# Performance work log

Measured on AMD Instinct MI355X. Metric: run time of the kernel, lower is better.

Reference implementation:

```python
import jax, jax.numpy as jnp
import numpy as np

B_SZ = 4; SEQ = 2048; D_INPUT = 40; D_MODEL = 128; N_LAYERS = 4
D_STATE = 16; EXPAND = 2; D_INNER = D_MODEL * EXPAND
N_HEADS = 4; D_HEAD = D_MODEL // N_HEADS; MAX_LANDMARKS = 100
EPS_RMS = 1.1920929e-07  # torch nn.RMSNorm default eps = finfo(float32).eps
EPS_LN = 1e-5
A_FLOOR = 1e-4


def _rms(x, w):
    return x * jax.lax.rsqrt(jnp.mean(x * x, -1, keepdims=True) + EPS_RMS) * w


def _ln(x, w, b):
    m = jnp.mean(x, -1, keepdims=True)
    v = jnp.mean((x - m) ** 2, -1, keepdims=True)
    return (x - m) * jax.lax.rsqrt(v + EPS_LN) * w + b


def _mamba3_block(xin, Wi, Wx, Wdt, bdt, Alog, Bb, Cb, Bnw, Cnw, rf, Dv, Wo):
    # xin: (B,L,d_model)
    xz = xin @ Wi                       # (B,L,2*d_inner)
    xp, z = jnp.split(xz, 2, axis=-1)
    xp = jax.nn.silu(xp)
    sp = xp @ Wx                        # (B,L,2*d_state+2)
    B_raw = sp[..., :D_STATE]
    C_raw = sp[..., D_STATE:2 * D_STATE]
    dt_in = sp[..., -2:-1]
    lam_in = sp[..., -1:]
    Bm = _rms(B_raw + Bb, Bnw)
    Cm = _rms(C_raw + Cb, Cnw)
    dt = jax.nn.softplus(dt_in @ Wdt + bdt)   # (B,L,d_inner)
    lam = jax.nn.sigmoid(lam_in)              # (B,L,1)
    # data-dependent RoPE on B and C
    freqs = jax.nn.softplus(rf)                                  # (d_state//2,)
    ang = jnp.cumsum(jnp.mean(dt, -1, keepdims=True), axis=1) * freqs  # (B,L,ds/2)
    ca, sa = jnp.cos(ang), jnp.sin(ang)

    def rot(M):
        e, o = M[..., ::2], M[..., 1::2]
        return jnp.stack([e * ca - o * sa, e * sa + o * ca], -1).reshape(M.shape)

    Bm, Cm = rot(Bm), rot(Cm)
    A = jnp.minimum(-jnp.exp(Alog), -A_FLOOR)   # (d_inner,d_state)
    dte = dt[..., None]                          # (B,L,d_inner,1)
    dA = jnp.exp(A * dte)                        # (B,L,d_inner,d_state)
    Bx = Bm[:, :, None, :] * xp[..., None]       # (B,L,d_inner,d_state)
    Bx_prev = jnp.concatenate([jnp.zeros_like(Bx[:, :1]), Bx[:, :-1]], axis=1)
    lame = lam[..., None]                        # (B,L,1,1)
    u = (1.0 - lame) * dte * dA * Bx_prev + lame * dte * Bx
    u = u.at[:, 0].set(dte[:, 0] * Bx[:, 0])     # t==0 case: h = dt*B*x (no lambda)

    def step(h, inp):
        dA_t, u_t, C_t = inp
        h = dA_t * h + u_t
        return h, jnp.sum(h * C_t[:, None, :], -1)

    h0 = jnp.zeros((xin.shape[0], D_INNER, D_STATE), xin.dtype)
    _, ys = jax.lax.scan(step, h0, (jnp.swapaxes(dA, 0, 1), jnp.swapaxes(u, 0, 1), jnp.swapaxes(Cm, 0, 1)))
    y = jnp.swapaxes(ys, 0, 1)                   # (B,L,d_inner)
    y = y + xp * Dv
    y = y * jax.nn.silu(z)
    return y @ Wo


def _landmark_attn(mo, skip, hw, WQ, bQ, WK, bK, WV, bV, WO, bO):
    Bsz, L, Dm = skip.shape
    k = min(MAX_LANDMARKS, L)
    _, idx = jax.lax.top_k(hw, k)
    idx = jnp.sort(idx, axis=1)                            # (B,k)
    kv = jnp.take_along_axis(skip, idx[..., None], axis=1)  # (B,k,Dm)
    q = mo[:, -1:, :]                                       # (B,1,Dm)
    Q = (q @ WQ + bQ).reshape(Bsz, 1, N_HEADS, D_HEAD).transpose(0, 2, 1, 3)
    K = (kv @ WK + bK).reshape(Bsz, k, N_HEADS, D_HEAD).transpose(0, 2, 1, 3)
    V = (kv @ WV + bV).reshape(Bsz, k, N_HEADS, D_HEAD).transpose(0, 2, 1, 3)
    scores = jnp.einsum('bhqd,bhkd->bhqk', Q, K) * (D_HEAD ** -0.5)
    probs = jax.nn.softmax(scores, axis=-1)
    out = jnp.einsum('bhqk,bhkd->bhqd', probs, V).transpose(0, 2, 1, 3).reshape(Bsz, Dm)
    return out @ WO + bO


def setup_inputs() -> dict:
    key = jax.random.key(0)
    ks = iter(jax.random.split(key, 64))

    def nrm(shape, s=0.02):
        return jax.random.normal(next(ks), shape, jnp.float32) * s

    nl, ds, di, dm = N_LAYERS, D_STATE, D_INNER, D_MODEL
    inp = {}
    inp['x'] = jax.random.normal(next(ks), (B_SZ, SEQ, D_INPUT), jnp.float32)
    inp['hawkes_weights'] = jax.random.uniform(next(ks), (B_SZ, SEQ), jnp.float32)
    inp['emb_W'] = nrm((D_INPUT, dm)); inp['emb_b'] = jnp.zeros(dm, jnp.float32)
    inp['skip_W'] = nrm((D_INPUT, dm)); inp['skip_b'] = jnp.zeros(dm, jnp.float32)
    inp['in_proj_W'] = nrm((nl, dm, 2 * di))
    inp['x_proj_W'] = nrm((nl, di, 2 * ds + 2))
    inp['dt_proj_W'] = nrm((nl, 1, di), 1.0)
    inp['dt_proj_b'] = jnp.full((nl, di), -1.0, jnp.float32)
    inp['A_log'] = jnp.broadcast_to(jnp.log(jnp.arange(1, ds + 1, dtype=jnp.float32)), (nl, di, ds)) * jnp.ones((nl, di, ds), jnp.float32)
    inp['B_bias'] = jnp.ones((nl, ds), jnp.float32)
    inp['C_bias'] = jnp.ones((nl, ds), jnp.float32)
    inp['Bn_w'] = jnp.ones((nl, ds), jnp.float32)
    inp['Cn_w'] = jnp.ones((nl, ds), jnp.float32)
    inp['rope_freqs'] = nrm((nl, ds // 2), 0.01)
    inp['D_param'] = jnp.ones((nl, di), jnp.float32)
    inp['out_proj_W'] = nrm((nl, di, dm))
    inp['ln_w'] = jnp.ones((nl, dm), jnp.float32); inp['ln_b'] = jnp.zeros((nl, dm), jnp.float32)
    inp['fn_w'] = jnp.ones(dm, jnp.float32); inp['fn_b'] = jnp.zeros(dm, jnp.float32)
    for nm in ('Q', 'K', 'V', 'O'):
        inp['W' + nm] = nrm((dm, dm)); inp['b' + nm] = jnp.zeros(dm, jnp.float32)
    return inp


def reference(x, hawkes_weights, emb_W, emb_b, skip_W, skip_b, in_proj_W, x_proj_W,
              dt_proj_W, dt_proj_b, A_log, B_bias, C_bias, Bn_w, Cn_w, rope_freqs,
              D_param, out_proj_W, ln_w, ln_b, fn_w, fn_b, WQ, bQ, WK, bK, WV, bV, WO, bO):
    w = hawkes_weights[..., None]
    h = (x @ emb_W + emb_b) * w          # Hawkes-damped embedding for Mamba path
    skip = (x @ skip_W + skip_b) * w     # Hawkes skip for attention KV
    for i in range(N_LAYERS):
        h = h + _mamba3_block(_ln(h, ln_w[i], ln_b[i]), in_proj_W[i], x_proj_W[i],
                              dt_proj_W[i], dt_proj_b[i], A_log[i], B_bias[i], C_bias[i],
                              Bn_w[i], Cn_w[i], rope_freqs[i], D_param[i], out_proj_W[i])
    mo = _ln(h, fn_w, fn_b)
    return _landmark_attn(mo, skip, hawkes_weights, WQ, bQ, WK, bK, WV, bV, WO, bO)
```

## Files before the change

### kernel.cpp

```cpp
#include <hip/hip_runtime.h>
#include <hip/hip_fp16.h>
#include <math.h>

#define BSZ   4
#define SEQL  2048
#define DIN   40
#define DM    128
#define DI    256
#define DS    16
#define NL    4
#define NHEAD 4
#define DHEAD 32
#define KLM   100
#define NC    128
#define TC    16
#define NROWS 8
#define EROWS 16

__device__ __forceinline__ float rcp_(float x){ return __builtin_amdgcn_rcpf(x); }
__device__ __forceinline__ float sigmoidf_(float x){ return rcp_(1.0f + __expf(-x)); }
__device__ __forceinline__ float siluf_(float x){ return x*rcp_(1.0f + __expf(-x)); }
__device__ __forceinline__ float softplusf_(float x){ return fmaxf(x,0.0f) + __logf(1.0f + __expf(-fabsf(x))); }

__device__ __forceinline__ void load8(const float* p, float* r){
  const float4* q = (const float4*)p;
  float4 a=q[0], b=q[1];
  r[0]=a.x;r[1]=a.y;r[2]=a.z;r[3]=a.w; r[4]=b.x;r[5]=b.y;r[6]=b.z;r[7]=b.w;
}
__device__ __forceinline__ void store8(float* p, const float* r){
  float4* q = (float4*)p;
  q[0]=make_float4(r[0],r[1],r[2],r[3]);  q[1]=make_float4(r[4],r[5],r[6],r[7]);
}
__device__ __forceinline__ void load16(const float* p, float* r){
  load8(p, r); load8(p+8, r+8);
}
__device__ __forceinline__ void store16(float* p, const float* r){
  store8(p, r); store8(p+8, r+8);
}

__global__ __launch_bounds__(256) void convw_kernel(
    const float* __restrict__ inW, const float* __restrict__ outW,
    __half* __restrict__ Wih, __half* __restrict__ Woh)
{
  const int i = blockIdx.x*256 + threadIdx.x;
  if (i < NL*DM*2*DI) Wih[i] = __float2half_rn(inW[i]);
  if (i < NL*DI*DM)   Woh[i] = __float2half_rn(outW[i]);
}

__global__ __launch_bounds__(256) void topk_kernel(
    const float* __restrict__ hw, int* __restrict__ idxl_g)
{
  __shared__ int redcnt[2][4];
  __shared__ int eqc[8][4], gtc[8][4];

  const int b = blockIdx.x;
  const int t = threadIdx.x;
  const int lane = t & 63, w = t >> 6;

  const float* hwp = hw + (size_t)b*SEQL;
  unsigned vb[8];
  #pragma unroll
  for (int q=0;q<8;q++) vb[q] = __float_as_uint(hwp[q*256 + t]);

  unsigned kth = 0u;
  for (int bit=31; bit>=0; --bit){
    const unsigned cand = kth | (1u << bit);
    int c0 = 0;
    #pragma unroll
    for (int q=0;q<8;q++) c0 += __popcll(__ballot(vb[q] >= cand));
    const int par = bit & 1;
    if (lane == 0) redcnt[par][w] = c0;
    __syncthreads();
    const int tot = redcnt[par][0]+redcnt[par][1]+redcnt[par][2]+redcnt[par][3];
    if (tot >= KLM) kth = cand;
  }

  unsigned long long beq[8], bgt[8];
  #pragma unroll
  for (int q=0;q<8;q++){
    beq[q] = __ballot(vb[q] == kth);
    bgt[q] = __ballot(vb[q] >  kth);
  }
  if (lane == 0){
    #pragma unroll
    for (int q=0;q<8;q++){ eqc[q][w] = __popcll(beq[q]); gtc[q][w] = __popcll(bgt[q]); }
  }
  __syncthreads();
  {
    int gtTot = 0;
    #pragma unroll
    for (int q=0;q<8;q++) gtTot += gtc[q][0]+gtc[q][1]+gtc[q][2]+gtc[q][3];
    const int need_eq = KLM - gtTot;
    const unsigned long long lmask = (lane==0) ? 0ull : ((~0ull) >> (64-lane));
    int eqPfx = 0, gtPfx = 0;
    #pragma unroll
    for (int q=0;q<8;q++){
      int eqWP = 0, gtWP = 0;
      for (int w2=0; w2<w; ++w2){ eqWP += eqc[q][w2]; gtWP += gtc[q][w2]; }
      const int eqBefore = eqPfx + eqWP + __popcll(beq[q] & lmask);
      const int gtBefore = gtPfx + gtWP + __popcll(bgt[q] & lmask);
      if (vb[q] > kth){
        const int pos = gtBefore + min(eqBefore, need_eq);
        if (pos < KLM) idxl_g[b*KLM + pos] = q*256 + t;
      } else if (vb[q] == kth && eqBefore < need_eq){
        const int pos = gtBefore + eqBefore;
        if (pos < KLM) idxl_g[b*KLM + pos] = q*256 + t;
      }
      eqPfx += eqc[q][0]+eqc[q][1]+eqc[q][2]+eqc[q][3];
      gtPfx += gtc[q][0]+gtc[q][1]+gtc[q][2]+gtc[q][3];
    }
  }
}

__global__ __launch_bounds__(256) void embed_kernel(
    const float* __restrict__ x, const float* __restrict__ hw,
    const float* __restrict__ eW, const float* __restrict__ eb,
    const float* __restrict__ sW, const float* __restrict__ sb,
    float* __restrict__ hb, float* __restrict__ sk)
{
  __shared__ float xr[EROWS][DIN];
  const int t = threadIdx.x;
  const size_t R0 = (size_t)blockIdx.x * EROWS;
  for (int e=t; e<EROWS*DIN; e+=256) ((float*)xr)[e] = x[R0*DIN + e];
  __syncthreads();
  const int c = t & (DM-1), g = t >> 7;
  float ae[8], as[8];
  #pragma unroll
  for (int j=0;j<8;j++){ ae[j]=0.0f; as[j]=0.0f; }
  for (int k=0;k<DIN;k++){
    const float we  = eW[(size_t)k*DM + c];
    const float ws_ = sW[(size_t)k*DM + c];
    #pragma unroll
    for (int j=0;j<8;j++){
      const float xv = xr[g*8+j][k];
      ae[j] = fmaf(xv, we, ae[j]);
      as[j] = fmaf(xv, ws_, as[j]);
    }
  }
  const float ebv = eb[c], sbv = sb[c];
  #pragma unroll
  for (int j=0;j<8;j++){
    const size_t R = R0 + g*8 + j;
    const float w = hw[R];
    hb[R*DM + c] = (ae[j]+ebv)*w;
    sk[R*DM + c] = (as[j]+sbv)*w;
  }
}

__global__ __launch_bounds__(256) void pre_kernel(
    const float* __restrict__ hb,
    const __half* __restrict__ Wih, const float* __restrict__ Wx,
    const float* __restrict__ Wdt, const float* __restrict__ bdt,
    const float* __restrict__ Bb, const float* __restrict__ Cb,
    const float* __restrict__ Bnw, const float* __restrict__ Cnw,
    const float* __restrict__ lnw, const float* __restrict__ lnb,
    __half* __restrict__ xph, __half* __restrict__ zsh,
    float* __restrict__ dtin, float* __restrict__ Shalf,
    float* __restrict__ Bmb, float* __restrict__ Cmb,
    float* __restrict__ lamb, float* __restrict__ mdtb)
{
  __shared__ float xin[NROWS][DM+4];
  __shared__ float xps[NROWS][DI+4];
  __shared__ float spl[NROWS][40];
  __shared__ float pr[NROWS][4];

  const int t = threadIdx.x;
  const size_t R0 = (size_t)blockIdx.x * NROWS;

  {
    const int r = t >> 5, j = t & 31;
    const float4 v = ((const float4*)(hb + (R0 + r)*DM))[j];
    float s = v.x+v.y+v.z+v.w;
    #pragma unroll
    for (int o=16;o>0;o>>=1) s += __shfl_xor(s,o,32);
    const float m = s*(1.0f/DM);
    const float dx=v.x-m, dy=v.y-m, dz=v.z-m, dw=v.w-m;
    float ss = dx*dx+dy*dy+dz*dz+dw*dw;
    #pragma unroll
    for (int o=16;o>0;o>>=1) ss += __shfl_xor(ss,o,32);
    const float inv = 1.0f/sqrtf(ss*(1.0f/DM) + 1e-5f);
    const int c = j*4;
    xin[r][c+0] = dx*inv*lnw[c+0] + lnb[c+0];
    xin[r][c+1] = dy*inv*lnw[c+1] + lnb[c+1];
    xin[r][c+2] = dz*inv*lnw[c+2] + lnb[c+2];
    xin[r][c+3] = dw*inv*lnw[c+3] + lnb[c+3];
  }
  __syncthreads();

  {
    float2 a[NROWS];
    #pragma unroll
    for (int r=0;r<NROWS;r++){ a[r].x=0.0f; a[r].y=0.0f; }
    const __half2* Wc = (const __half2*)Wih + t;
    for (int k=0;k<DM;k+=4){
      const float2 w0 = __half22float2(Wc[(size_t)(k+0)*(DI)]);
      const float2 w1 = __half22float2(Wc[(size_t)(k+1)*(DI)]);
      const float2 w2 = __half22float2(Wc[(size_t)(k+2)*(DI)]);
      const float2 w3 = __half22float2(Wc[(size_t)(k+3)*(DI)]);
      #pragma unroll
      for (int r=0;r<NROWS;r++){
        const float4 xv = *(const float4*)&xin[r][k];
        a[r].x = fmaf(xv.x,w0.x,a[r].x); a[r].y = fmaf(xv.x,w0.y,a[r].y);
        a[r].x = fmaf(xv.y,w1.x,a[r].x); a[r].y = fmaf(xv.y,w1.y,a[r].y);
        a[r].x = fmaf(xv.z,w2.x,a[r].x); a[r].y = fmaf(xv.z,w2.y,a[r].y);
        a[r].x = fmaf(xv.w,w3.x,a[r].x); a[r].y = fmaf(xv.w,w3.y,a[r].y);
      }
    }
    if (t < 128){
      #pragma unroll
      for (int r=0;r<NROWS;r++){
        const float sx = siluf_(a[r].x), sy = siluf_(a[r].y);
        xps[r][2*t] = sx; xps[r][2*t+1] = sy;
        *(__half2*)&xph[(R0+r)*DI + 2*t] =
            __halves2half2(__float2half_rn(sx), __float2half_rn(sy));
      }
    } else {
      const int zc = 2*t - 2*DI + DI;
      #pragma unroll
      for (int r=0;r<NROWS;r++){
        const float sx = siluf_(a[r].x), sy = siluf_(a[r].y);
        *(__half2*)&zsh[(R0+r)*DI + zc] =
            __halves2half2(__float2half_rn(sx), __float2half_rn(sy));
      }
    }
  }
  __syncthreads();

  if (t < 136){
    const int r = t & 7, op = t >> 3;
    float ax=0.0f, ay=0.0f;
    for (int k=0;k<DI;k+=4){
      const float4 xv = *(const float4*)&xps[r][k];
      const float2 w0 = *(const float2*)&Wx[(size_t)(k+0)*34 + 2*op];
      const float2 w1 = *(const float2*)&Wx[(size_t)(k+1)*34 + 2*op];
      const float2 w2 = *(const float2*)&Wx[(size_t)(k+2)*34 + 2*op];
      const float2 w3 = *(const float2*)&Wx[(size_t)(k+3)*34 + 2*op];
      ax = fmaf(xv.x,w0.x,ax); ay = fmaf(xv.x,w0.y,ay);
      ax = fmaf(xv.y,w1.x,ax); ay = fmaf(xv.y,w1.y,ay);
      ax = fmaf(xv.z,w2.x,ax); ay = fmaf(xv.z,w2.y,ay);
      ax = fmaf(xv.w,w3.x,ax); ay = fmaf(xv.w,w3.y,ay);
    }
    spl[r][2*op] = ax; spl[r][2*op+1] = ay;
  }
  __syncthreads();

  {
    const int half = t >> 7;
    const int r2 = (t >> 4) & 7, s2 = t & 15;
    const float* bias = half ? Cb : Bb;
    const float* wn   = half ? Cnw : Bnw;
    const float v = spl[r2][half*DS + s2] + bias[s2];
    float ss = v*v;
    #pragma unroll
    for (int o=8;o>0;o>>=1) ss += __shfl_xor(ss,o,16);
    const float inv = 1.0f/sqrtf(ss*(1.0f/DS) + 1.1920929e-07f);
    (half ? Cmb : Bmb)[(R0+r2)*DS + s2] = v*inv*wn[s2];
  }

  {
    const int lane = t & 63, w = t >> 6;
    const float wdt = Wdt[t], bdtv = bdt[t];
    float Sd = 0.0f;
    #pragma unroll
    for (int r=0;r<NROWS;r++){
      const float dval = softplusf_(fmaf(spl[r][32], wdt, bdtv));
      Sd += dval;
      float s = dval;
      #pragma unroll
      for (int o=32;o>0;o>>=1) s += __shfl_xor(s,o,64);
      if (lane==0) pr[r][w] = s;
    }
    Shalf[(size_t)blockIdx.x * DI + t] = Sd;
    if (t < NROWS){
      lamb[R0+t] = sigmoidf_(spl[t][33]);
      dtin[R0+t] = spl[t][32];
    }
  }
  __syncthreads();
  if (t < NROWS)
    mdtb[R0+t] = (pr[t][0]+pr[t][1]+pr[t][2]+pr[t][3])*(1.0f/DI);
}

__global__ __launch_bounds__(256) void cumsum_kernel(
    const float* __restrict__ mdt, double* __restrict__ csum_g)
{
  __shared__ double wsum[4];
  const int b = blockIdx.x, t = threadIdx.x;
  const int lane = t & 63, w = t >> 6;
  const float* p = mdt + (size_t)b*SEQL + (size_t)t*8;
  double v[8]; double s = 0.0;
  #pragma unroll
  for (int q=0;q<8;q++){ v[q] = (double)p[q]; s += v[q]; }
  double sc = s;
  #pragma unroll
  for (int o=1;o<64;o<<=1){
    const double nb = __shfl_up(sc, o, 64);
    if (lane >= o) sc += nb;
  }
  if (lane==63) wsum[w] = sc;
  __syncthreads();
  double woff = 0.0;
  for (int j=0;j<w;j++) woff += wsum[j];
  double run = woff + sc - s;
  double* dst = csum_g + (size_t)b*SEQL + (size_t)t*8;
  #pragma unroll
  for (int q=0;q<8;q++){ run += v[q]; dst[q] = run; }
}

__global__ __launch_bounds__(256) void csfill_kernel(
    const double* __restrict__ csum_g, const float* __restrict__ rf,
    float2* __restrict__ cst)
{
  __shared__ double fqs[8];
  const int t = threadIdx.x;
  if (t < 8){
    const double xfr = (double)rf[t];
    fqs[t] = fmax(xfr, 0.0) + log1p(exp(-fabs(xfr)));
  }
  __syncthreads();
  const int row = blockIdx.x*256 + t;
  const double ab = csum_g[row];
  const double TWO_PI = 6.283185307179586;
  const double INV2PI = 0.15915494309189535;
  float2 o8[8];
  #pragma unroll
  for (int f=0; f<8; f++){
    const double ang = ab * fqs[f];
    const double red = ang - floor(ang*INV2PI)*TWO_PI;
    float sa, ca;
    __sincosf((float)red, &sa, &ca);
    o8[f] = make_float2(ca, sa);
  }
  float4* dst = (float4*)&cst[(size_t)row*8];
  dst[0] = make_float4(o8[0].x,o8[0].y,o8[1].x,o8[1].y);
  dst[1] = make_float4(o8[2].x,o8[2].y,o8[3].x,o8[3].y);
  dst[2] = make_float4(o8[4].x,o8[4].y,o8[5].x,o8[5].y);
  dst[3] = make_float4(o8[6].x,o8[6].y,o8[7].x,o8[7].y);
}

__global__ __launch_bounds__(512) void scan1_kernel(
    const __half* __restrict__ xph, const float* __restrict__ dtin,
    const float* __restrict__ Wdt, const float* __restrict__ bdt,
    const float* __restrict__ Bmb, const float* __restrict__ lamb,
    const float2* __restrict__ cst,
    const float* __restrict__ Alog, float* __restrict__ hend)
{
  __shared__ float Bst[TC+1][DS];
  __shared__ float lst[TC];
  __shared__ float dsl[TC];
  __shared__ __half xpl[TC+1][DI+8];
  const int t = threadIdx.x;
  const int d  = t >> 1;
  const int s0 = (t & 1) * 8;
  const int c = blockIdx.x & (NC-1);
  const int b = blockIdx.x >> 7;
  const size_t bL = (size_t)b*SEQL;
  const int t0 = c*TC;
  const int id = blockIdx.x*256 + d;

  for (int e=t; e<(TC+1)*DS; e+=512){
    const int j = e >> 4, s = e & 15;
    const int trow = t0 - 1 + j;
    Bst[j][s] = (trow >= 0) ? Bmb[(bL + trow)*DS + s] : 0.0f;
  }
  for (int e=t; e<(TC+1)*DI; e+=512){
    const int j = e >> 8, dd = e & (DI-1);
    const int trow = t0 - 1 + j;
    xpl[j][dd] = (trow >= 0) ? xph[(bL + trow)*DI + dd] : __float2half_rn(0.0f);
  }
  if (t < TC){
    lst[t] = lamb[bL + t0 + t];
    dsl[t] = dtin[bL + t0 + t];
  }
  __syncthreads();
  if (t < 136){
    const int j = t >> 3, f = t & 7;
    const int trow = t0 - 1 + j;
    if (trow >= 0){
      const float2 cs = cst[((size_t)(bL + trow))*8 + f];
      const float e0 = Bst[j][2*f], o0 = Bst[j][2*f+1];
      Bst[j][2*f]   = e0*cs.x - o0*cs.y;
      Bst[j][2*f+1] = e0*cs.y + o0*cs.x;
    }
  }
  __syncthreads();

  float A[8];
  #pragma unroll
  for (int s=0;s<8;s++) A[s] = fminf(-__expf(Alog[d*DS + s0 + s]), -1e-4f);
  const float wdt = Wdt[d], bdtv = bdt[d];
  float h[8], Bprev[8];
  #pragma unroll
  for (int s=0;s<8;s++) h[s]=0.0f;
  float xpm1;
  int tstart;
  if (t0 > 0){
    #pragma unroll
    for (int s=0;s<8;s++) Bprev[s] = Bst[0][s0+s];
    xpm1 = __half2float(xpl[0][d]);
    tstart = 0;
  } else {
    const float dtv = softplusf_(fmaf(dsl[0], wdt, bdtv));
    const float xpv = __half2float(xpl[1][d]);
    #pragma unroll
    for (int s=0;s<8;s++){
      h[s] = dtv*(Bst[1][s0+s]*xpv);
      Bprev[s] = Bst[1][s0+s];
    }
    xpm1 = xpv;
    tstart = 1;
  }
  for (int j=tstart; j<TC; ++j){
    const float dtv = softplusf_(fmaf(dsl[j], wdt, bdtv));
    const float xpv = __half2float(xpl[j+1][d]);
    const float lamv = lst[j];
    const float dl = dtv*lamv;
    const float dml = dtv - dl;
    #pragma unroll
    for (int s=0;s<8;s++){
      const float a = __expf(A[s]*dtv);
      const float Bc = Bst[j+1][s0+s];
      const float u = fmaf(dml*a, Bprev[s]*xpm1, dl*(Bc*xpv));
      h[s] = fmaf(a, h[s], u);
      Bprev[s] = Bc;
    }
    xpm1 = xpv;
  }
  store8(hend + (size_t)id*DS + s0, h);
}

__global__ __launch_bounds__(128) void scan2_kernel(
    float* __restrict__ hend, const float* __restrict__ Shalf,
    const float* __restrict__ Alog)
{
  __shared__ float hS[NC][DS+1];
  __shared__ float pS[NC][DS+1];
  const int c = threadIdx.x;
  const int d = blockIdx.x & (DI-1);
  const int b = blockIdx.x >> 8;
  const float S = Shalf[(size_t)(b*(SEQL/NROWS) + 2*c)*DI + d]
                + Shalf[(size_t)(b*(SEQL/NROWS) + 2*c + 1)*DI + d];
  float P[DS], h[DS];
  #pragma unroll
  for (int s=0;s<DS;s++){
    const float A = fminf(-__expf(Alog[d*DS+s]), -1e-4f);
    P[s] = __expf(A*S);
  }
  load16(hend + (((size_t)(b*NC + c))*DI + d)*DS, h);
  #pragma unroll
  for (int s=0;s<DS;s++){ hS[c][s]=h[s]; pS[c][s]=P[s]; }
  __syncthreads();
  for (int off=1; off<NC; off<<=1){
    float hn[DS], pn[DS];
    const int src = c - off;
    if (src >= 0){
      #pragma unroll
      for (int s=0;s<DS;s++){ hn[s]=hS[src][s]; pn[s]=pS[src][s]; }
    }
    __syncthreads();
    if (src >= 0){
      #pragma unroll
      for (int s=0;s<DS;s++){
        h[s] = fmaf(P[s], hn[s], h[s]);
        P[s] *= pn[s];
        hS[c][s] = h[s]; pS[c][s] = P[s];
      }
    }
    __syncthreads();
  }
  float o[DS];
  if (c == 0){
    #pragma unroll
    for (int s=0;s<DS;s++) o[s] = 0.0f;
  } else {
    #pragma unroll
    for (int s=0;s<DS;s++) o[s] = hS[c-1][s];
  }
  store16(hend + (((size_t)(b*NC + c))*DI + d)*DS, o);
}

__global__ __launch_bounds__(512) void scan3post_kernel(
    const __half* __restrict__ xph, const float* __restrict__ dtin,
    const float* __restrict__ Wdt, const float* __restrict__ bdt,
    const float* __restrict__ Bmb, const float* __restrict__ Cmb,
    const float* __restrict__ lamb, const __half* __restrict__ zsh,
    const float2* __restrict__ cst,
    const float* __restrict__ Alog, const float* __restrict__ Dv,
    const float* __restrict__ Hin, const __half* __restrict__ Woh,
    float* __restrict__ hb)
{
  __shared__ float Bst[TC+1][DS];
  __shared__ float Cst[TC][DS];
  __shared__ float lst[TC];
  __shared__ float dsl[TC];
  __shared__ __half xpl[TC+1][DI+8];
  __shared__ __half zsl[TC][DI+8];
  __shared__ float ys[TC][DI+4];
  const int t = threadIdx.x;
  const int d  = t >> 1;
  const int sh = t & 1;
  const int s0 = sh * 8;
  const int c = blockIdx.x & (NC-1);
  const int b = blockIdx.x >> 7;
  const size_t bL = (size_t)b*SEQL;
  const int t0 = c*TC;
  const int id = blockIdx.x*256 + d;

  for (int e=t; e<(TC+1)*DS; e+=512){
    const int j = e >> 4, s = e & 15;
    const int trow = t0 - 1 + j;
    Bst[j][s] = (trow >= 0) ? Bmb[(bL + trow)*DS + s] : 0.0f;
    if (j < TC) Cst[j][s] = Cmb[(bL + t0 + j)*DS + s];
  }
  for (int e=t; e<(TC+1)*DI; e+=512){
    const int j = e >> 8, dd = e & (DI-1);
    const int trow = t0 - 1 + j;
    xpl[j][dd] = (trow >= 0) ? xph[(bL + trow)*DI + dd] : __float2half_rn(0.0f);
    if (j < TC) zsl[j][dd] = zsh[(bL + t0 + j)*DI + dd];
  }
  if (t < TC){
    lst[t] = lamb[bL + t0 + t];
    dsl[t] = dtin[bL + t0 + t];
  }
  __syncthreads();
  if (t < 264){
    if (t < 136){
      const int j = t >> 3, f = t & 7;
      const int trow = t0 - 1 + j;
      if (trow >= 0){
        const float2 cs = cst[((size_t)(bL + trow))*8 + f];
        const float e0 = Bst[j][2*f], o0 = Bst[j][2*f+1];
        Bst[j][2*f]   = e0*cs.x - o0*cs.y;
        Bst[j][2*f+1] = e0*cs.y + o0*cs.x;
      }
    } else {
      const int e2 = t - 136;
      const int j = e2 >> 3, f = e2 & 7;
      const float2 cs = cst[((size_t)(bL + t0 + j))*8 + f];
      const float e0 = Cst[j][2*f], o0 = Cst[j][2*f+1];
      Cst[j][2*f]   = e0*cs.x - o0*cs.y;
      Cst[j][2*f+1] = e0*cs.y + o0*cs.x;
    }
  }
  __syncthreads();

  float A[8];
  #pragma unroll
  for (int s=0;s<8;s++) A[s] = fminf(-__expf(Alog[d*DS + s0 + s]), -1e-4f);
  const float wdt = Wdt[d], bdtv = bdt[d];
  const float dvp = Dv[d];
  float h[8], Bprev[8];
  load8(Hin + (size_t)id*DS + s0, h);
  float xpm1;
  int tstart;
  if (t0 > 0){
    #pragma unroll
    for (int s=0;s<8;s++) Bprev[s] = Bst[0][s0+s];
    xpm1 = __half2float(xpl[0][d]);
    tstart = 0;
  } else {
    const float dtv = softplusf_(fmaf(dsl[0], wdt, bdtv));
    const float xpv = __half2float(xpl[1][d]);
    float y = 0.0f;
    #pragma unroll
    for (int s=0;s<8;s++){
      h[s] = dtv*(Bst[1][s0+s]*xpv);
      y = fmaf(h[s], Cst[0][s0+s], y);
      Bprev[s] = Bst[1][s0+s];
    }
    const float ytot = y + __shfl_xor(y, 1, 64);
    if (sh == 0) ys[0][d] = (ytot + xpv*dvp)*__half2float(zsl[0][d]);
    xpm1 = xpv;
    tstart = 1;
  }
  for (int j=tstart; j<TC; ++j){
    const float dtv = softplusf_(fmaf(dsl[j], wdt, bdtv));
    const float xpv = __half2float(xpl[j+1][d]);
    const float lamv = lst[j];
    const float dl = dtv*lamv;
    const float dml = dtv - dl;
    float y = 0.0f;
    #pragma unroll
    for (int s=0;s<8;s++){
      const float a = __expf(A[s]*dtv);
      const float Bc = Bst[j+1][s0+s];
      const float u = fmaf(dml*a, Bprev[s]*xpm1, dl*(Bc*xpv));
      h[s] = fmaf(a, h[s], u);
      y = fmaf(h[s], Cst[j][s0+s], y);
      Bprev[s] = Bc;
    }
    const float ytot = y + __shfl_xor(y, 1, 64);
    if (sh == 0) ys[j][d] = (ytot + xpv*dvp)*__half2float(zsl[j][d]);
    xpm1 = xpv;
  }
  __syncthreads();

  {
    const int cg2  = t & 31;
    const int ks2  = (t >> 5) & 1;
    const int rg   = (t >> 6) & 3;
    const int ksHi = t >> 8;
    const int seg = ksHi*2 + ks2;
    const int k0 = seg*64;
    const int c0c = cg2*4;
    float acc[4][4];
    #pragma unroll
    for (int rr=0;rr<4;rr++){ acc[rr][0]=0.f; acc[rr][1]=0.f; acc[rr][2]=0.f; acc[rr][3]=0.f; }
    for (int k=k0; k<k0+64; k+=4){
      float4 yv[4];
      #pragma unroll
      for (int rr=0;rr<4;rr++) yv[rr] = *(const float4*)&ys[rg*4+rr][k];
      #pragma unroll
      for (int j=0;j<4;j++){
        const float2 wlo = __half22float2(*(const __half2*)&Woh[(size_t)(k+j)*DM + c0c]);
        const float2 whi = __half22float2(*(const __half2*)&Woh[(size_t)(k+j)*DM + c0c + 2]);
        const float y0 = (j==0)?yv[0].x:(j==1)?yv[0].y:(j==2)?yv[0].z:yv[0].w;
        const float y1 = (j==0)?yv[1].x:(j==1)?yv[1].y:(j==2)?yv[1].z:yv[1].w;
        const float y2 = (j==0)?yv[2].x:(j==1)?yv[2].y:(j==2)?yv[2].z:yv[2].w;
        const float y3 = (j==0)?yv[3].x:(j==1)?yv[3].y:(j==2)?yv[3].z:yv[3].w;
        acc[0][0]=fmaf(y0,wlo.x,acc[0][0]); acc[0][1]=fmaf(y0,wlo.y,acc[0][1]);
        acc[0][2]=fmaf(y0,whi.x,acc[0][2]); acc[0][3]=fmaf(y0,whi.y,acc[0][3]);
        acc[1][0]=fmaf(y1,wlo.x,acc[1][0]); acc[1][1]=fmaf(y1,wlo.y,acc[1][1]);
        acc[1][2]=fmaf(y1,whi.x,acc[1][2]); acc[1][3]=fmaf(y1,whi.y,acc[1][3]);
        acc[2][0]=fmaf(y2,wlo.x,acc[2][0]); acc[2][1]=fmaf(y2,wlo.y,acc[2][1]);
        acc[2][2]=fmaf(y2,whi.x,acc[2][2]); acc[2][3]=fmaf(y2,whi.y,acc[2][3]);
        acc[3][0]=fmaf(y3,wlo.x,acc[3][0]); acc[3][1]=fmaf(y3,wlo.y,acc[3][1]);
        acc[3][2]=fmaf(y3,whi.x,acc[3][2]); acc[3][3]=fmaf(y3,whi.y,acc[3][3]);
      }
    }
    #pragma unroll
    for (int rr=0;rr<4;rr++){
      #pragma unroll
      for (int cc=0;cc<4;cc++) acc[rr][cc] += __shfl_down(acc[rr][cc], 32, 64);
    }
    float (*red)[132] = (float(*)[132])ys;
    __syncthreads();
    const int lane = t & 63;
    if (ksHi == 1 && lane < 32){
      #pragma unroll
      for (int rr=0;rr<4;rr++)
        *(float4*)&red[rg*4+rr][c0c] = make_float4(acc[rr][0],acc[rr][1],acc[rr][2],acc[rr][3]);
    }
    __syncthreads();
    if (ksHi == 0 && lane < 32){
      #pragma unroll
      for (int rr=0;rr<4;rr++){
        const float4 rv = *(const float4*)&red[rg*4+rr][c0c];
        const size_t row = bL + t0 + rg*4 + rr;
        float4 hv = *(const float4*)&hb[row*DM + c0c];
        hv.x += acc[rr][0] + rv.x; hv.y += acc[rr][1] + rv.y;
        hv.z += acc[rr][2] + rv.z; hv.w += acc[rr][3] + rv.w;
        *(float4*)&hb[row*DM + c0c] = hv;
      }
    }
  }
}

__global__ __launch_bounds__(256) void attnmid_kernel(
    const float* __restrict__ hb, const float* __restrict__ sk,
    const int* __restrict__ idxl_g,
    const float* __restrict__ fnw, const float* __restrict__ fnb,
    const float* __restrict__ WQ, const float* __restrict__ bQ,
    const float* __restrict__ WK, const float* __restrict__ bK,
    const float* __restrict__ WV, const float* __restrict__ bV,
    float* __restrict__ attnog)
{
  __shared__ float kv[KLM][DM+4];
  __shared__ float mo[DM];
  __shared__ float Qs[DHEAD];
  __shared__ float qk[DM];
  __shared__ float sc[KLM];
  __shared__ float pbar[DM];
  __shared__ float bterm_s;
  const int t = threadIdx.x;
  const int b = blockIdx.x >> 2, hh = blockIdx.x & 3;
  const int c0 = hh*DHEAD;

  if (t < 64){
    const float* hr = hb + ((size_t)b*SEQL + (SEQL-1))*DM;
    const float v0 = hr[t], v1 = hr[t+64];
    float s = v0+v1;
    #pragma unroll
    for (int o=32;o>0;o>>=1) s += __shfl_xor(s,o,64);
    const float m = s*(1.0f/DM);
    const float d0=v0-m, d1=v1-m;
    float ss = d0*d0 + d1*d1;
    #pragma unroll
    for (int o=32;o>0;o>>=1) ss += __shfl_xor(ss,o,64);
    const float inv = 1.0f/sqrtf(ss*(1.0f/DM) + 1e-5f);
    mo[t]    = d0*inv*fnw[t]    + fnb[t];
    mo[t+64] = d1*inv*fnw[t+64] + fnb[t+64];
  }
  for (int e=t; e<KLM*DM; e+=256){
    const int j = e >> 7, cc = e & (DM-1);
    kv[j][cc] = sk[((size_t)b*SEQL + idxl_g[b*KLM + j])*DM + cc];
  }
  __syncthreads();
  if (t < DHEAD){
    float a = bQ[c0+t];
    #pragma unroll 4
    for (int k=0;k<DM;k++) a = fmaf(mo[k], WQ[(size_t)k*DM + c0+t], a);
// ... 65 lines not shown
  __syncthreads();
  float a = bO[t];
  #pragma unroll 4
  for (int c2=0;c2<DM;c2++) a = fmaf(ao[c2], WO[(size_t)c2*DM + t], a);
  outp[(size_t)b*DM + t] = a;
}

extern "C" void kernel_launch(void* const* d_in, const int* in_sizes, int n_in,
                              void* d_out, int out_size, void* d_ws, size_t ws_size,
                              hipStream_t stream)
{
  (void)in_sizes; (void)n_in; (void)out_size; (void)ws_size;
  const float* x    = (const float*)d_in[0];
  const float* hw   = (const float*)d_in[1];
  const float* embW = (const float*)d_in[2];
  const float* embB = (const float*)d_in[3];
  const float* skW  = (const float*)d_in[4];
  const float* skB  = (const float*)d_in[5];
  const float* inW  = (const float*)d_in[6];
  const float* xpW  = (const float*)d_in[7];
  const float* dtW  = (const float*)d_in[8];
  const float* dtB  = (const float*)d_in[9];
  const float* Alog = (const float*)d_in[10];
  const float* Bb   = (const float*)d_in[11];
  const float* Cb   = (const float*)d_in[12];
  const float* Bnw  = (const float*)d_in[13];
  const float* Cnw  = (const float*)d_in[14];
  const float* rf   = (const float*)d_in[15];
  const float* Dpar = (const float*)d_in[16];
  const float* outW = (const float*)d_in[17];
  const float* lnW  = (const float*)d_in[18];
  const float* lnB  = (const float*)d_in[19];
  const float* fnW  = (const float*)d_in[20];
  const float* fnB  = (const float*)d_in[21];
  const float* WQ = (const float*)d_in[22]; const float* bQ = (const float*)d_in[23];
  const float* WK = (const float*)d_in[24]; const float* bK = (const float*)d_in[25];
  const float* WV = (const float*)d_in[26]; const float* bV = (const float*)d_in[27];
  const float* WO = (const float*)d_in[28]; const float* bO = (const float*)d_in[29];

  float* ws = (float*)d_ws;
  size_t off = 0;
  float* hb    = ws + off; off += (size_t)BSZ*SEQL*DM;
  float* sk    = ws + off; off += (size_t)BSZ*SEQL*DM;
  __half* xph  = (__half*)(ws + off); off += (size_t)BSZ*SEQL*DI/2;
  __half* zsh  = (__half*)(ws + off); off += (size_t)BSZ*SEQL*DI/2;
  float* Bmb   = ws + off; off += (size_t)BSZ*SEQL*DS;
  float* Cmb   = ws + off; off += (size_t)BSZ*SEQL*DS;
  float* lamb  = ws + off; off += (size_t)BSZ*SEQL;
  float* mdtb  = ws + off; off += (size_t)BSZ*SEQL;
  float* dtin  = ws + off; off += (size_t)BSZ*SEQL;
  float* Shalf = ws + off; off += (size_t)BSZ*(SEQL/NROWS)*DI;
  float* hend  = ws + off; off += (size_t)BSZ*NC*DI*DS;
  float2* cst  = (float2*)(ws + off); off += (size_t)BSZ*SEQL*16;
  double* csum_g = (double*)(ws + off); off += (size_t)BSZ*SEQL*2;
  int* idxl_g  = (int*)(ws + off); off += (size_t)BSZ*KLM;
  float* attnog= ws + off; off += (size_t)BSZ*DM;
  __half* Wih  = (__half*)(ws + off); off += (size_t)NL*DM*2*DI/2;
  __half* Woh  = (__half*)(ws + off); off += (size_t)NL*DI*DM/2;

  convw_kernel<<<(NL*DM*2*DI + 255)/256, 256, 0, stream>>>(inW, outW, Wih, Woh);
  topk_kernel<<<BSZ, 256, 0, stream>>>(hw, idxl_g);
  embed_kernel<<<BSZ*SEQL/EROWS, 256, 0, stream>>>(x, hw, embW, embB, skW, skB, hb, sk);

  for (int i=0;i<NL;i++){
    pre_kernel<<<BSZ*SEQL/NROWS, 256, 0, stream>>>(hb,
        Wih + (size_t)i*DM*2*DI, xpW + (size_t)i*DI*34,
        dtW + (size_t)i*DI, dtB + (size_t)i*DI,
        Bb + i*DS, Cb + i*DS, Bnw + i*DS, Cnw + i*DS,
        lnW + i*DM, lnB + i*DM,
        xph, zsh, dtin, Shalf, Bmb, Cmb, lamb, mdtb);
    cumsum_kernel<<<BSZ, 256, 0, stream>>>(mdtb, csum_g);
    csfill_kernel<<<BSZ*SEQL/256, 256, 0, stream>>>(csum_g, rf + i*8, cst);
    scan1_kernel<<<BSZ*NC, 512, 0, stream>>>(xph, dtin,
        dtW + (size_t)i*DI, dtB + (size_t)i*DI,
        Bmb, lamb, cst, Alog + (size_t)i*DI*DS, hend);
    scan2_kernel<<<BSZ*DI, 128, 0, stream>>>(hend, Shalf, Alog + (size_t)i*DI*DS);
    scan3post_kernel<<<BSZ*NC, 512, 0, stream>>>(xph, dtin,
        dtW + (size_t)i*DI, dtB + (size_t)i*DI,
        Bmb, Cmb, lamb, zsh, cst,
        Alog + (size_t)i*DI*DS, Dpar + (size_t)i*DI, hend,
        Woh + (size_t)i*DI*DM, hb);
  }

  attnmid_kernel<<<BSZ*NHEAD, 256, 0, stream>>>(hb, sk, idxl_g, fnW, fnB,
      WQ, bQ, WK, bK, WV, bV, attnog);
  attnout_kernel<<<BSZ, 128, 0, stream>>>(attnog, WO, bO, (float*)d_out);
}
```

Baseline: 515.1 us.

## Halve scan chunk length to double chunk parallelism and fuse cumsum with sincos fill

Scan chunks shrink from 16 to 8 timesteps and the chunk count doubles to 256, so scan1/scan3 launch twice as many blocks and each does a shorter sequential recurrence. scan2 now runs 256 threads over the longer chunk prefix and reads Shalf directly at one entry per chunk, and the out-projection in scan3post is retiled to 2 rows per thread group. Separately, the cumsum and cos/sin fill kernels are merged into one kernel that keeps the cumulative sum in shared memory, removing a launch and the global double buffer. The cost is a deeper cross-chunk scan in scan2, more hend traffic, and the fused trig fill now running on only 4 blocks.

Result: slower. 543.4 us (+5.5%).

```diff
diff --git a/kernel.cpp b/kernel.cpp
--- a/kernel.cpp
+++ b/kernel.cpp
@@ -12,8 +12,8 @@
 #define NHEAD 4
 #define DHEAD 32
 #define KLM   100
-#define NC    128
-#define TC    16
+#define NC    256
+#define TC    8
 #define NROWS 8
 #define EROWS 16
 
@@ -281,12 +281,19 @@
     mdtb[R0+t] = (pr[t][0]+pr[t][1]+pr[t][2]+pr[t][3])*(1.0f/DI);
 }
 
-__global__ __launch_bounds__(256) void cumsum_kernel(
-    const float* __restrict__ mdt, double* __restrict__ csum_g)
-{
+__global__ __launch_bounds__(256) void cumcs_kernel(
+    const float* __restrict__ mdt, const float* __restrict__ rf,
+    float2* __restrict__ cst)
+{
+  __shared__ double csum[SEQL];
   __shared__ double wsum[4];
+  __shared__ double fqs[8];
   const int b = blockIdx.x, t = threadIdx.x;
   const int lane = t & 63, w = t >> 6;
+  if (t < 8){
+    const double xfr = (double)rf[t];
+    fqs[t] = fmax(xfr, 0.0) + log1p(exp(-fabs(xfr)));
+  }
   const float* p = mdt + (size_t)b*SEQL + (size_t)t*8;
   double v[8]; double s = 0.0;
   #pragma unroll
@@ -302,40 +309,30 @@
   double woff = 0.0;
   for (int j=0;j<w;j++) woff += wsum[j];
   double run = woff + sc - s;
-  double* dst = csum_g + (size_t)b*SEQL + (size_t)t*8;
-  #pragma unroll
-  for (int q=0;q<8;q++){ run += v[q]; dst[q] = run; }
-}
-
-__global__ __launch_bounds__(256) void csfill_kernel(
-    const double* __restrict__ csum_g, const float* __restrict__ rf,
-    float2* __restrict__ cst)
-{
-  __shared__ double fqs[8];
-  const int t = threadIdx.x;
-  if (t < 8){
-    const double xfr = (double)rf[t];
-    fqs[t] = fmax(xfr, 0.0) + log1p(exp(-fabs(xfr)));
-  }
-  __syncthreads();
-  const int row = blockIdx.x*256 + t;
-  const double ab = csum_g[row];
+  #pragma unroll
+  for (int q=0;q<8;q++){ run += v[q]; csum[t*8+q] = run; }
+  __syncthreads();
+
   const double TWO_PI = 6.283185307179586;
   const double INV2PI = 0.15915494309189535;
-  float2 o8[8];
-  #pragma unroll
-  for (int f=0; f<8; f++){
-    const double ang = ab * fqs[f];
-    const double red = ang - floor(ang*INV2PI)*TWO_PI;
-    float sa, ca;
-    __sincosf((float)red, &sa, &ca);
-    o8[f] = make_float2(ca, sa);
-  }
-  float4* dst = (float4*)&cst[(size_t)row*8];
-  dst[0] = make_float4(o8[0].x,o8[0].y,o8[1].x,o8[1].y);
-  dst[1] = make_float4(o8[2].x,o8[2].y,o8[3].x,o8[3].y);
-  dst[2] = make_float4(o8[4].x,o8[4].y,o8[5].x,o8[5].y);
-  dst[3] = make_float4(o8[6].x,o8[6].y,o8[7].x,o8[7].y);
+  for (int j=0;j<8;j++){
+    const int rloc = j*256 + t;
+    const double ab = csum[rloc];
+    float2 o8[8];
+    #pragma unroll
+    for (int f=0; f<8; f++){
+      const double ang = ab * fqs[f];
+      const double red = ang - floor(ang*INV2PI)*TWO_PI;
+      float sa, ca;
+      __sincosf((float)red, &sa, &ca);
+      o8[f] = make_float2(ca, sa);
+    }
+    float4* dst = (float4*)&cst[((size_t)b*SEQL + rloc)*8];
+    dst[0] = make_float4(o8[0].x,o8[0].y,o8[1].x,o8[1].y);
+    dst[1] = make_float4(o8[2].x,o8[2].y,o8[3].x,o8[3].y);
+    dst[2] = make_float4(o8[4].x,o8[4].y,o8[5].x,o8[5].y);
+    dst[3] = make_float4(o8[6].x,o8[6].y,o8[7].x,o8[7].y);
+  }
 }
 
 __global__ __launch_bounds__(512) void scan1_kernel(
@@ -353,13 +350,13 @@
   const int d  = t >> 1;
   const int s0 = (t & 1) * 8;
   const int c = blockIdx.x & (NC-1);
-  const int b = blockIdx.x >> 7;
+  const int b = blockIdx.x >> 8;
   const size_t bL = (size_t)b*SEQL;
   const int t0 = c*TC;
   const int id = blockIdx.x*256 + d;
 
-  for (int e=t; e<(TC+1)*DS; e+=512){
-    const int j = e >> 4, s = e & 15;
+  if (t < (TC+1)*DS){
+    const int j = t >> 4, s = t & 15;
     const int trow = t0 - 1 + j;
     Bst[j][s] = (trow >= 0) ? Bmb[(bL + trow)*DS + s] : 0.0f;
   }
@@ -373,7 +370,7 @@
     dsl[t] = dtin[bL + t0 + t];
   }
   __syncthreads();
-  if (t < 136){
+  if (t < (TC+1)*8){
     const int j = t >> 3, f = t & 7;
     const int trow = t0 - 1 + j;
     if (trow >= 0){
@@ -429,7 +426,7 @@
   store8(hend + (size_t)id*DS + s0, h);
 }
 
-__global__ __launch_bounds__(128) void scan2_kernel(
+__global__ __launch_bounds__(256) void scan2_kernel(
     float* __restrict__ hend, const float* __restrict__ Shalf,
     const float* __restrict__ Alog)
 {
@@ -438,8 +435,7 @@
   const int c = threadIdx.x;
   const int d = blockIdx.x & (DI-1);
   const int b = blockIdx.x >> 8;
-  const float S = Shalf[(size_t)(b*(SEQL/NROWS) + 2*c)*DI + d]
-                + Shalf[(size_t)(b*(SEQL/NROWS) + 2*c + 1)*DI + d];
+  const float S = Shalf[((size_t)(b*NC + c))*DI + d];
   float P[DS], h[DS];
   #pragma unroll
   for (int s=0;s<DS;s++){
@@ -501,13 +497,13 @@
   const int sh = t & 1;
   const int s0 = sh * 8;
   const int c = blockIdx.x & (NC-1);
-  const int b = blockIdx.x >> 7;
+  const int b = blockIdx.x >> 8;
   const size_t bL = (size_t)b*SEQL;
   const int t0 = c*TC;
   const int id = blockIdx.x*256 + d;
 
-  for (int e=t; e<(TC+1)*DS; e+=512){
-    const int j = e >> 4, s = e & 15;
+  if (t < (TC+1)*DS){
+    const int j = t >> 4, s = t & 15;
     const int trow = t0 - 1 + j;
     Bst[j][s] = (trow >= 0) ? Bmb[(bL + trow)*DS + s] : 0.0f;
     if (j < TC) Cst[j][s] = Cmb[(bL + t0 + j)*DS + s];
@@ -523,8 +519,8 @@
     dsl[t] = dtin[bL + t0 + t];
   }
   __syncthreads();
-  if (t < 264){
-    if (t < 136){
+  if (t < (TC+1)*8 + TC*8){
+    if (t < (TC+1)*8){
       const int j = t >> 3, f = t & 7;
       const int trow = t0 - 1 + j;
       if (trow >= 0){
@@ -534,7 +530,7 @@
         Bst[j][2*f+1] = e0*cs.y + o0*cs.x;
       }
     } else {
-      const int e2 = t - 136;
+      const int e2 = t - (TC+1)*8;
       const int j = e2 >> 3, f = e2 & 7;
       const float2 cs = cst[((size_t)(bL + t0 + j))*8 + f];
       const float e0 = Cst[j][2*f], o0 = Cst[j][2*f+1];
@@ -596,57 +592,51 @@
   __syncthreads();
 
   {
-    const int cg2  = t & 31;
-    const int ks2  = (t >> 5) & 1;
-    const int rg   = (t >> 6) & 3;
-    const int ksHi = t >> 8;
-    const int seg = ksHi*2 + ks2;
+    const int cg2 = t & 31;
+    const int ksl = (t >> 5) & 1;
+    const int ksh = (t >> 6) & 1;
+    const int rg  = (t >> 7) & 3;
+    const int seg = ksh*2 + ksl;
     const int k0 = seg*64;
     const int c0c = cg2*4;
-    float acc[4][4];
-    #pragma unroll
-    for (int rr=0;rr<4;rr++){ acc[rr][0]=0.f; acc[rr][1]=0.f; acc[rr][2]=0.f; acc[rr][3]=0.f; }
+    float acc[2][4];
+    #pragma unroll
+    for (int rr=0;rr<2;rr++){ acc[rr][0]=0.f; acc[rr][1]=0.f; acc[rr][2]=0.f; acc[rr][3]=0.f; }
     for (int k=k0; k<k0+64; k+=4){
-      float4 yv[4];
-      #pragma unroll
-      for (int rr=0;rr<4;rr++) yv[rr] = *(const float4*)&ys[rg*4+rr][k];
+      float4 yv[2];
+      #pragma unroll
+      for (int rr=0;rr<2;rr++) yv[rr] = *(const float4*)&ys[rg*2+rr][k];
       #pragma unroll
       for (int j=0;j<4;j++){
         const float2 wlo = __half22float2(*(const __half2*)&Woh[(size_t)(k+j)*DM + c0c]);
         const float2 whi = __half22float2(*(const __half2*)&Woh[(size_t)(k+j)*DM + c0c + 2]);
         const float y0 = (j==0)?yv[0].x:(j==1)?yv[0].y:(j==2)?yv[0].z:yv[0].w;
         const float y1 = (j==0)?yv[1].x:(j==1)?yv[1].y:(j==2)?yv[1].z:yv[1].w;
-        const float y2 = (j==0)?yv[2].x:(j==1)?yv[2].y:(j==2)?yv[2].z:yv[2].w;
-        const float y3 = (j==0)?yv[3].x:(j==1)?yv[3].y:(j==2)?yv[3].z:yv[3].w;
         acc[0][0]=fmaf(y0,wlo.x,acc[0][0]); acc[0][1]=fmaf(y0,wlo.y,acc[0][1]);
         acc[0][2]=fmaf(y0,whi.x,acc[0][2]); acc[0][3]=fmaf(y0,whi.y,acc[0][3]);
         acc[1][0]=fmaf(y1,wlo.x,acc[1][0]); acc[1][1]=fmaf(y1,wlo.y,acc[1][1]);
         acc[1][2]=fmaf(y1,whi.x,acc[1][2]); acc[1][3]=fmaf(y1,whi.y,acc[1][3]);
-        acc[2][0]=fmaf(y2,wlo.x,acc[2][0]); acc[2][1]=fmaf(y2,wlo.y,acc[2][1]);
-        acc[2][2]=fmaf(y2,whi.x,acc[2][2]); acc[2][3]=fmaf(y2,whi.y,acc[2][3]);
-        acc[3][0]=fmaf(y3,wlo.x,acc[3][0]); acc[3][1]=fmaf(y3,wlo.y,acc[3][1]);
-        acc[3][2]=fmaf(y3,whi.x,acc[3][2]); acc[3][3]=fmaf(y3,whi.y,acc[3][3]);
       }
     }
     #pragma unroll
-    for (int rr=0;rr<4;rr++){
+    for (int rr=0;rr<2;rr++){
       #pragma unroll
       for (int cc=0;cc<4;cc++) acc[rr][cc] += __shfl_down(acc[rr][cc], 32, 64);
     }
     float (*red)[132] = (float(*)[132])ys;
     __syncthreads();
     const int lane = t & 63;
-    if (ksHi == 1 && lane < 32){
-      #pragma unroll
-      for (int rr=0;rr<4;rr++)
-        *(float4*)&red[rg*4+rr][c0c] = make_float4(acc[rr][0],acc[rr][1],acc[rr][2],acc[rr][3]);
+    if (ksh == 1 && lane < 32){
+      #pragma unroll
+      for (int rr=0;rr<2;rr++)
+        *(float4*)&red[rg*2+rr][c0c] = make_float4(acc[rr][0],acc[rr][1],acc[rr][2],acc[rr][3]);
     }
     __syncthreads();
-    if (ksHi == 0 && lane < 32){
-      #pragma unroll
-      for (int rr=0;rr<4;rr++){
-        const float4 rv = *(const float4*)&red[rg*4+rr][c0c];
-        const size_t row = bL + t0 + rg*4 + rr;
+    if (ksh == 0 && lane < 32){
+      #pragma unroll
+      for (int rr=0;rr<2;rr++){
+        const float4 rv = *(const float4*)&red[rg*2+rr][c0c];
+        const size_t row = bL + t0 + rg*2 + rr;
         float4 hv = *(const float4*)&hb[row*DM + c0c];
         hv.x += acc[rr][0] + rv.x; hv.y += acc[rr][1] + rv.y;
         hv.z += acc[rr][2] + rv.z; hv.w += acc[rr][3] + rv.w;
@@ -818,7 +808,6 @@
   float* Shalf = ws + off; off += (size_t)BSZ*(SEQL/NROWS)*DI;
   float* hend  = ws + off; off += (size_t)BSZ*NC*DI*DS;
   float2* cst  = (float2*)(ws + off); off += (size_t)BSZ*SEQL*16;
-  double* csum_g = (double*)(ws + off); off += (size_t)BSZ*SEQL*2;
   int* idxl_g  = (int*)(ws + off); off += (size_t)BSZ*KLM;
   float* attnog= ws + off; off += (size_t)BSZ*DM;
   __half* Wih  = (__half*)(ws + off); off += (size_t)NL*DM*2*DI/2;
@@ -835,12 +824,11 @@
         Bb + i*DS, Cb + i*DS, Bnw + i*DS, Cnw + i*DS,
         lnW + i*DM, lnB + i*DM,
         xph, zsh, dtin, Shalf, Bmb, Cmb, lamb, mdtb);
-    cumsum_kernel<<<BSZ, 256, 0, stream>>>(mdtb, csum_g);
-    csfill_kernel<<<BSZ*SEQL/256, 256, 0, stream>>>(csum_g, rf + i*8, cst);
+    cumcs_kernel<<<BSZ, 256, 0, stream>>>(mdtb, rf + i*8, cst);
     scan1_kernel<<<BSZ*NC, 512, 0, stream>>>(xph, dtin,
         dtW + (size_t)i*DI, dtB + (size_t)i*DI,
         Bmb, lamb, cst, Alog + (size_t)i*DI*DS, hend);
-    scan2_kernel<<<BSZ*DI, 128, 0, stream>>>(hend, Shalf, Alog + (size_t)i*DI*DS);
+    scan2_kernel<<<BSZ*DI, 256, 0, stream>>>(hend, Shalf, Alog + (size_t)i*DI*DS);
     scan3post_kernel<<<BSZ*NC, 512, 0, stream>>>(xph, dtin,
         dtW + (size_t)i*DI, dtB + (size_t)i*DI,
         Bmb, Cmb, lamb, zsh, cst,
```

## Use fp16 dot2 for in_proj, repack weights by k-pairs, fuse cumsum with sincos fill

Applied to the files above, without the earlier changes.

The in_proj GEMV in pre_kernel now keeps the layernormed input in shared memory as half2 and uses v_dot2 (fdot2) with weights repacked into k-pair interleaved layout, so one 8-byte load feeds two output columns. This halves the FMA instruction count and the number of weight loads. The cumsum and csfill kernels are merged into one per-batch kernel that keeps the prefix sum in shared memory, which removes a launch and a global double round trip per layer. The trade-offs are lower precision from fp16 activations in the dot, and only 4 blocks doing all the sincos work.

Result: no change. 507.4 us (-1.5%).

```diff
diff --git a/kernel.cpp b/kernel.cpp
--- a/kernel.cpp
+++ b/kernel.cpp
@@ -17,10 +17,15 @@
 #define NROWS 8
 #define EROWS 16
 
+typedef _Float16 v2h __attribute__((ext_vector_type(2)));
+
 __device__ __forceinline__ float rcp_(float x){ return __builtin_amdgcn_rcpf(x); }
 __device__ __forceinline__ float sigmoidf_(float x){ return rcp_(1.0f + __expf(-x)); }
 __device__ __forceinline__ float siluf_(float x){ return x*rcp_(1.0f + __expf(-x)); }
 __device__ __forceinline__ float softplusf_(float x){ return fmaxf(x,0.0f) + __logf(1.0f + __expf(-fabsf(x))); }
+__device__ __forceinline__ float fdot2_(__half2 a, __half2 b, float c){
+  return __builtin_amdgcn_fdot2(*(v2h*)&a, *(v2h*)&b, c, false);
+}
 
 __device__ __forceinline__ void load8(const float* p, float* r){
   const float4* q = (const float4*)p;
@@ -40,11 +45,16 @@
 
 __global__ __launch_bounds__(256) void convw_kernel(
     const float* __restrict__ inW, const float* __restrict__ outW,
-    __half* __restrict__ Wih, __half* __restrict__ Woh)
+    __half* __restrict__ Wip, __half* __restrict__ Woh)
 {
   const int i = blockIdx.x*256 + threadIdx.x;
-  if (i < NL*DM*2*DI) Wih[i] = __float2half_rn(inW[i]);
-  if (i < NL*DI*DM)   Woh[i] = __float2half_rn(outW[i]);
+  if (i < NL*DM*2*DI){
+    const int col = i & 511;
+    const int klin = i >> 9;
+    const int l = klin >> 7, k = klin & 127;
+    Wip[(((size_t)(l*64 + (k>>1))*512 + col) << 1) + (k & 1)] = __float2half_rn(inW[i]);
+  }
+  if (i < NL*DI*DM) Woh[i] = __float2half_rn(outW[i]);
 }
 
 __global__ __launch_bounds__(256) void topk_kernel(
@@ -149,7 +159,7 @@
 
 __global__ __launch_bounds__(256) void pre_kernel(
     const float* __restrict__ hb,
-    const __half* __restrict__ Wih, const float* __restrict__ Wx,
+    const __half* __restrict__ Wip, const float* __restrict__ Wx,
     const float* __restrict__ Wdt, const float* __restrict__ bdt,
     const float* __restrict__ Bb, const float* __restrict__ Cb,
     const float* __restrict__ Bnw, const float* __restrict__ Cnw,
@@ -159,7 +169,7 @@
     float* __restrict__ Bmb, float* __restrict__ Cmb,
     float* __restrict__ lamb, float* __restrict__ mdtb)
 {
-  __shared__ float xin[NROWS][DM+4];
+  __shared__ __half2 xinh[NROWS][64+2];
   __shared__ float xps[NROWS][DI+4];
   __shared__ float spl[NROWS][40];
   __shared__ float pr[NROWS][4];
@@ -180,10 +190,12 @@
     for (int o=16;o>0;o>>=1) ss += __shfl_xor(ss,o,32);
     const float inv = 1.0f/sqrtf(ss*(1.0f/DM) + 1e-5f);
     const int c = j*4;
-    xin[r][c+0] = dx*inv*lnw[c+0] + lnb[c+0];
-    xin[r][c+1] = dy*inv*lnw[c+1] + lnb[c+1];
-    xin[r][c+2] = dz*inv*lnw[c+2] + lnb[c+2];
-    xin[r][c+3] = dw*inv*lnw[c+3] + lnb[c+3];
+    const float v0 = dx*inv*lnw[c+0] + lnb[c+0];
+    const float v1 = dy*inv*lnw[c+1] + lnb[c+1];
+    const float v2 = dz*inv*lnw[c+2] + lnb[c+2];
+    const float v3 = dw*inv*lnw[c+3] + lnb[c+3];
+    xinh[r][2*j]   = __halves2half2(__float2half_rn(v0), __float2half_rn(v1));
+    xinh[r][2*j+1] = __halves2half2(__float2half_rn(v2), __float2half_rn(v3));
   }
   __syncthreads();
 
@@ -191,19 +203,17 @@
     float2 a[NROWS];
     #pragma unroll
     for (int r=0;r<NROWS;r++){ a[r].x=0.0f; a[r].y=0.0f; }
-    const __half2* Wc = (const __half2*)Wih + t;
-    for (int k=0;k<DM;k+=4){
-      const float2 w0 = __half22float2(Wc[(size_t)(k+0)*(DI)]);
-      const float2 w1 = __half22float2(Wc[(size_t)(k+1)*(DI)]);
-      const float2 w2 = __half22float2(Wc[(size_t)(k+2)*(DI)]);
-      const float2 w3 = __half22float2(Wc[(size_t)(k+3)*(DI)]);
+    const __half2* Wc = (const __half2*)Wip + 2*t;
+    #pragma unroll 4
+    for (int p=0;p<64;p++){
+      const float2 wv = *(const float2*)&Wc[(size_t)p*512];
+      const __half2 w0 = *(const __half2*)&wv.x;
+      const __half2 w1 = *(const __half2*)&wv.y;
       #pragma unroll
       for (int r=0;r<NROWS;r++){
-        const float4 xv = *(const float4*)&xin[r][k];
-        a[r].x = fmaf(xv.x,w0.x,a[r].x); a[r].y = fmaf(xv.x,w0.y,a[r].y);
-        a[r].x = fmaf(xv.y,w1.x,a[r].x); a[r].y = fmaf(xv.y,w1.y,a[r].y);
-        a[r].x = fmaf(xv.z,w2.x,a[r].x); a[r].y = fmaf(xv.z,w2.y,a[r].y);
-        a[r].x = fmaf(xv.w,w3.x,a[r].x); a[r].y = fmaf(xv.w,w3.y,a[r].y);
+        const __half2 xv = xinh[r][p];
+        a[r].x = fdot2_(xv, w0, a[r].x);
+        a[r].y = fdot2_(xv, w1, a[r].y);
       }
     }
     if (t < 128){
@@ -281,12 +291,19 @@
     mdtb[R0+t] = (pr[t][0]+pr[t][1]+pr[t][2]+pr[t][3])*(1.0f/DI);
 }
 
-__global__ __launch_bounds__(256) void cumsum_kernel(
-    const float* __restrict__ mdt, double* __restrict__ csum_g)
-{
+__global__ __launch_bounds__(256) void cumcs_kernel(
+    const float* __restrict__ mdt, const float* __restrict__ rf,
+    float2* __restrict__ cst)
+{
+  __shared__ double csum[SEQL];
   __shared__ double wsum[4];
+  __shared__ double fqs[8];
   const int b = blockIdx.x, t = threadIdx.x;
   const int lane = t & 63, w = t >> 6;
+  if (t < 8){
+    const double xfr = (double)rf[t];
+    fqs[t] = fmax(xfr, 0.0) + log1p(exp(-fabs(xfr)));
+  }
   const float* p = mdt + (size_t)b*SEQL + (size_t)t*8;
   double v[8]; double s = 0.0;
   #pragma unroll
@@ -302,40 +319,30 @@
   double woff = 0.0;
   for (int j=0;j<w;j++) woff += wsum[j];
   double run = woff + sc - s;
-  double* dst = csum_g + (size_t)b*SEQL + (size_t)t*8;
-  #pragma unroll
-  for (int q=0;q<8;q++){ run += v[q]; dst[q] = run; }
-}
-
-__global__ __launch_bounds__(256) void csfill_kernel(
-    const double* __restrict__ csum_g, const float* __restrict__ rf,
-    float2* __restrict__ cst)
-{
-  __shared__ double fqs[8];
-  const int t = threadIdx.x;
-  if (t < 8){
-    const double xfr = (double)rf[t];
-    fqs[t] = fmax(xfr, 0.0) + log1p(exp(-fabs(xfr)));
-  }
-  __syncthreads();
-  const int row = blockIdx.x*256 + t;
-  const double ab = csum_g[row];
+  #pragma unroll
+  for (int q=0;q<8;q++){ run += v[q]; csum[t*8+q] = run; }
+  __syncthreads();
+
   const double TWO_PI = 6.283185307179586;
   const double INV2PI = 0.15915494309189535;
-  float2 o8[8];
-  #pragma unroll
-  for (int f=0; f<8; f++){
-    const double ang = ab * fqs[f];
-    const double red = ang - floor(ang*INV2PI)*TWO_PI;
-    float sa, ca;
-    __sincosf((float)red, &sa, &ca);
-    o8[f] = make_float2(ca, sa);
-  }
-  float4* dst = (float4*)&cst[(size_t)row*8];
-  dst[0] = make_float4(o8[0].x,o8[0].y,o8[1].x,o8[1].y);
-  dst[1] = make_float4(o8[2].x,o8[2].y,o8[3].x,o8[3].y);
-  dst[2] = make_float4(o8[4].x,o8[4].y,o8[5].x,o8[5].y);
-  dst[3] = make_float4(o8[6].x,o8[6].y,o8[7].x,o8[7].y);
+  for (int j=0;j<8;j++){
+    const int rloc = j*256 + t;
+    const double ab = csum[rloc];
+    float2 o8[8];
+    #pragma unroll
+    for (int f=0; f<8; f++){
+      const double ang = ab * fqs[f];
+      const double red = ang - floor(ang*INV2PI)*TWO_PI;
+      float sa, ca;
+      __sincosf((float)red, &sa, &ca);
+      o8[f] = make_float2(ca, sa);
+    }
+    float4* dst = (float4*)&cst[((size_t)b*SEQL + rloc)*8];
+    dst[0] = make_float4(o8[0].x,o8[0].y,o8[1].x,o8[1].y);
+    dst[1] = make_float4(o8[2].x,o8[2].y,o8[3].x,o8[3].y);
+    dst[2] = make_float4(o8[4].x,o8[4].y,o8[5].x,o8[5].y);
+    dst[3] = make_float4(o8[6].x,o8[6].y,o8[7].x,o8[7].y);
+  }
 }
 
 __global__ __launch_bounds__(512) void scan1_kernel(
@@ -818,25 +825,23 @@
   float* Shalf = ws + off; off += (size_t)BSZ*(SEQL/NROWS)*DI;
   float* hend  = ws + off; off += (size_t)BSZ*NC*DI*DS;
   float2* cst  = (float2*)(ws + off); off += (size_t)BSZ*SEQL*16;
-  double* csum_g = (double*)(ws + off); off += (size_t)BSZ*SEQL*2;
   int* idxl_g  = (int*)(ws + off); off += (size_t)BSZ*KLM;
   float* attnog= ws + off; off += (size_t)BSZ*DM;
-  __half* Wih  = (__half*)(ws + off); off += (size_t)NL*DM*2*DI/2;
+  __half* Wip  = (__half*)(ws + off); off += (size_t)NL*DM*2*DI/2;
   __half* Woh  = (__half*)(ws + off); off += (size_t)NL*DI*DM/2;
 
-  convw_kernel<<<(NL*DM*2*DI + 255)/256, 256, 0, stream>>>(inW, outW, Wih, Woh);
+  convw_kernel<<<(NL*DM*2*DI + 255)/256, 256, 0, stream>>>(inW, outW, Wip, Woh);
   topk_kernel<<<BSZ, 256, 0, stream>>>(hw, idxl_g);
   embed_kernel<<<BSZ*SEQL/EROWS, 256, 0, stream>>>(x, hw, embW, embB, skW, skB, hb, sk);
 
   for (int i=0;i<NL;i++){
     pre_kernel<<<BSZ*SEQL/NROWS, 256, 0, stream>>>(hb,
-        Wih + (size_t)i*DM*2*DI, xpW + (size_t)i*DI*34,
+        Wip + (size_t)i*DM*2*DI, xpW + (size_t)i*DI*34,
         dtW + (size_t)i*DI, dtB + (size_t)i*DI,
         Bb + i*DS, Cb + i*DS, Bnw + i*DS, Cnw + i*DS,
         lnW + i*DM, lnB + i*DM,
         xph, zsh, dtin, Shalf, Bmb, Cmb, lamb, mdtb);
-    cumsum_kernel<<<BSZ, 256, 0, stream>>>(mdtb, csum_g);
-    csfill_kernel<<<BSZ*SEQL/256, 256, 0, stream>>>(csum_g, rf + i*8, cst);
+    cumcs_kernel<<<BSZ, 256, 0, stream>>>(mdtb, rf + i*8, cst);
     scan1_kernel<<<BSZ*NC, 512, 0, stream>>>(xph, dtin,
         dtW + (size_t)i*DI, dtB + (size_t)i*DI,
         Bmb, lamb, cst, Alog + (size_t)i*DI*DS, hend);
```
